# Kernel tuning notes

Hardware: AMD Instinct MI355X
Metric: run time of the kernel (lower is better)

## Reference

```python
import jax, jax.numpy as jnp
import numpy as np
from jax import lax

NPOINT = 1024
RADIUS = 0.4
NSAMPLE = 32
BN_EPS = 1e-5


def _square_distance(src, dst):
    # src [B,S,3], dst [B,N,3] -> [B,S,N]
    d = -2.0 * jnp.einsum('bsc,bnc->bsn', src, dst)
    d = d + jnp.sum(src ** 2, -1)[:, :, None]
    d = d + jnp.sum(dst ** 2, -1)[:, None, :]
    return d


def _farthest_point_sample(xyz, npoint):
    # xyz [B,N,3] -> int32 indices [B,npoint]
    B, N, _ = xyz.shape
    # deterministic start at index 0 (torch uses randint; math is otherwise identical)
    init_far = jnp.zeros((B,), dtype=jnp.int32)
    init_dist = jnp.full((B, N), 1e10, dtype=xyz.dtype)

    def step(carry, _):
        distance, farthest = carry
        centroid = jnp.take_along_axis(xyz, farthest[:, None, None], axis=1)  # [B,1,3]
        dist = jnp.sum((xyz - centroid) ** 2, -1)  # [B,N]
        distance = jnp.minimum(distance, dist)
        new_far = jnp.argmax(distance, axis=-1).astype(jnp.int32)
        return (distance, new_far), farthest

    (_, _), cents = lax.scan(step, (init_dist, init_far), None, length=npoint)
    return cents.T  # [B, npoint]


def _query_ball_point(radius, nsample, xyz, new_xyz):
    # xyz [B,N,3], new_xyz [B,S,3] -> idx [B,S,nsample]
    B, N, _ = xyz.shape
    sqr = _square_distance(new_xyz, xyz)  # [B,S,N]
    ar = jnp.arange(N, dtype=jnp.int32)
    gi = jnp.where(sqr > radius * radius, N, ar[None, None, :])
    gi = jnp.sort(gi, axis=-1)[:, :, :nsample]
    first = gi[:, :, :1]
    return jnp.where(gi == N, first, gi)


def setup_inputs() -> dict:
    key = jax.random.key(0)
    ks = jax.random.split(key, 8)
    B, N = 16, 4096
    inp = {
        'xyz': jax.random.normal(ks[0], (B, 3, N), jnp.float32),
        'points': jax.random.normal(ks[1], (B, 6, N), jnp.float32),
    }
    dims = [(64, 9), (64, 64), (128, 64)]
    for i, (o, c) in enumerate(dims):
        inp[f'w{i}'] = jax.random.normal(ks[2 + i], (o, c), jnp.float32) * 0.05
        inp[f'b{i}'] = jnp.zeros((o,), jnp.float32)
        inp[f'g{i}'] = jnp.ones((o,), jnp.float32)
        inp[f'beta{i}'] = jnp.zeros((o,), jnp.float32)
    return inp


def reference(xyz, points, w0, b0, g0, beta0, w1, b1, g1, beta1, w2, b2, g2, beta2):
    # xyz [B,3,N], points [B,6,N]
    xyz_t = jnp.transpose(xyz, (0, 2, 1))      # [B,N,3]
    pts_t = jnp.transpose(points, (0, 2, 1))   # [B,N,6]
    B, N, _ = xyz_t.shape
    S, ns = NPOINT, NSAMPLE

    fps_idx = _farthest_point_sample(xyz_t, S)                 # [B,S]
    new_xyz = jnp.take_along_axis(xyz_t, fps_idx[:, :, None], axis=1)  # [B,S,3]
    idx = _query_ball_point(RADIUS, ns, xyz_t, new_xyz)        # [B,S,ns]
    flat = idx.reshape(B, S * ns, 1)
    g_xyz = jnp.take_along_axis(xyz_t, flat, axis=1).reshape(B, S, ns, 3)
    g_xyz = g_xyz - new_xyz[:, :, None, :]                     # grouped_xyz_norm
    g_pts = jnp.take_along_axis(pts_t, flat, axis=1).reshape(B, S, ns, -1)
    feat = jnp.concatenate([g_xyz, g_pts], axis=-1)            # [B,S,ns,9]

    # shared MLP: 1x1 conv + BatchNorm (training-mode batch stats) + ReLU
    for w, b, g, be in ((w0, b0, g0, beta0), (w1, b1, g1, beta1), (w2, b2, g2, beta2)):
        h = jnp.einsum('bsnc,oc->bsno', feat, w) + b
        mu = jnp.mean(h, axis=(0, 1, 2))
        var = jnp.var(h, axis=(0, 1, 2))
        feat = jax.nn.relu((h - mu) * lax.rsqrt(var + BN_EPS) * g + be)

    new_points = jnp.max(feat, axis=2)                         # max over nsample -> [B,S,Cout]
    return (jnp.transpose(new_xyz, (0, 2, 1)), jnp.transpose(new_points, (0, 2, 1)))
```

## Files before the change

kernel.cpp:

```cpp
#include <hip/hip_runtime.h>
#include <hip/hip_bf16.h>
#include <stdint.h>

#define NB 16
#define NP 4096
#define NSP 1024
#define KNN 32
#define PTOT (NB*NSP*KNN)
#define NTILES (PTOT/16)

typedef __attribute__((ext_vector_type(8))) short short8;
typedef __attribute__((ext_vector_type(4))) float f32x4;
typedef __attribute__((ext_vector_type(2))) float f32x2;

__device__ __forceinline__ float fadd_(float a,float b){return __fadd_rn(a,b);}
__device__ __forceinline__ float fmul_(float a,float b){return __fmul_rn(a,b);}
__device__ __forceinline__ float fsub_(float a,float b){return __fsub_rn(a,b);}

__device__ __forceinline__ float bf2f(unsigned short u){
    unsigned int x = ((unsigned int)u) << 16; float f; __builtin_memcpy(&f,&x,4); return f;
}
__device__ __forceinline__ unsigned short f2bf(float f){
    unsigned int x; __builtin_memcpy(&x,&f,4);
    x = x + 0x7fffu + ((x>>16)&1u);
    return (unsigned short)(x>>16);
}

template<int CTRL>
__device__ __forceinline__ unsigned long long dpp_max_step(unsigned long long v){
    unsigned int lo = (unsigned int)v, hi = (unsigned int)(v>>32);
    unsigned int lod = (unsigned int)__builtin_amdgcn_update_dpp(0, (int)lo, CTRL, 0xF, 0xF, true);
    unsigned int hid = (unsigned int)__builtin_amdgcn_update_dpp(0, (int)hi, CTRL, 0xF, 0xF, true);
    unsigned long long o = ((unsigned long long)hid<<32) | lod;
    return (o > v) ? o : v;
}

__global__ __launch_bounds__(512,1) void fps_kernel(const float* __restrict__ xyz,
    int* __restrict__ fps_idx)
{
    const int b = blockIdx.x, tid = threadIdx.x;
    const int lane = tid & 63, wv = tid >> 6;
    const float* xb = xyz + (size_t)b*3*NP;
    __shared__ float4 sp[NP];
    __shared__ unsigned long long slots[2][8];
    f32x2 px[4], py[4], pz[4];
    float pd[8];
    const int base = tid*8;
#pragma unroll
    for (int j=0;j<8;j+=4){
        float4 vx = *(const float4*)(xb + base + j);
        float4 vy = *(const float4*)(xb + NP + base + j);
        float4 vz = *(const float4*)(xb + 2*NP + base + j);
        px[j/2]   = (f32x2){vx.x,vx.y}; px[j/2+1] = (f32x2){vx.z,vx.w};
        py[j/2]   = (f32x2){vy.x,vy.y}; py[j/2+1] = (f32x2){vy.z,vy.w};
        pz[j/2]   = (f32x2){vz.x,vz.y}; pz[j/2+1] = (f32x2){vz.z,vz.w};
        sp[base+j+0] = make_float4(vx.x,vy.x,vz.x,0.f);
        sp[base+j+1] = make_float4(vx.y,vy.y,vz.y,0.f);
        sp[base+j+2] = make_float4(vx.z,vy.z,vz.z,0.f);
        sp[base+j+3] = make_float4(vx.w,vy.w,vz.w,0.f);
        pd[j]=1e10f; pd[j+1]=1e10f; pd[j+2]=1e10f; pd[j+3]=1e10f;
    }
    __syncthreads();
    int far = 0;
    float cx, cy, cz;
    { float4 c0 = sp[0]; cx=c0.x; cy=c0.y; cz=c0.z; }
    for (int s=0;s<NSP;s++){
        if (tid==0) fps_idx[b*NSP+s] = far;
        float bd=-1.0f; int bi=0;
        {
#pragma clang fp contract(off)
            const f32x2 cx2 = (f32x2){cx,cx}, cy2 = (f32x2){cy,cy}, cz2 = (f32x2){cz,cz};
#pragma unroll
            for (int k=0;k<4;k++){
                f32x2 dx = px[k]-cx2, dy = py[k]-cy2, dz = pz[k]-cz2;
                f32x2 d  = (dx*dx + dy*dy) + dz*dz;
                float nd0 = fminf(pd[2*k],   d.x);
                float nd1 = fminf(pd[2*k+1], d.y);
                pd[2*k]=nd0; pd[2*k+1]=nd1;
                if (nd0 > bd){ bd=nd0; bi=base+2*k;   }
                if (nd1 > bd){ bd=nd1; bi=base+2*k+1; }
            }
        }
        unsigned int hb; __builtin_memcpy(&hb,&bd,4);
        unsigned long long best = ((unsigned long long)hb<<32) | (unsigned int)(NP-1-bi);
        best = dpp_max_step<0x111>(best);
        best = dpp_max_step<0x112>(best);
        best = dpp_max_step<0x114>(best);
        best = dpp_max_step<0x118>(best);
        best = dpp_max_step<0x142>(best);
        best = dpp_max_step<0x143>(best);
        if (lane==63) slots[s&1][wv] = best;
        __syncthreads();
        {
            const unsigned long long* sl = slots[s&1];
            unsigned long long a0 = sl[0], a1 = sl[1], a2 = sl[2], a3 = sl[3];
            unsigned long long a4 = sl[4], a5 = sl[5], a6 = sl[6], a7 = sl[7];
            unsigned long long m0 = a0>a1?a0:a1, m1 = a2>a3?a2:a3;
            unsigned long long m2 = a4>a5?a4:a5, m3 = a6>a7?a6:a7;
            unsigned long long n0 = m0>m1?m0:m1, n1 = m2>m3?m2:m3;
            unsigned long long m  = n0>n1?n0:n1;
            far = NP-1-(int)(m & 0xFFFFFFFFu);
        }
        float4 c = sp[far]; cx=c.x; cy=c.y; cz=c.z;
    }
}

__global__ void centroid_kernel(const float* __restrict__ xyz, const int* __restrict__ fps_idx,
    float* __restrict__ new_xyz, float* __restrict__ out0)
{
    int t = blockIdx.x*256 + threadIdx.x;
    if (t >= NB*NSP) return;
    int b = t>>10, s = t&1023;
    int id = fps_idx[t];
    const float* xb = xyz + (size_t)b*3*NP;
    float x=xb[id], y=xb[NP+id], z=xb[2*NP+id];
    float* nz = new_xyz + (size_t)t*3;
    nz[0]=x; nz[1]=y; nz[2]=z;
    out0[(size_t)b*3*NSP + s]         = x;
    out0[(size_t)b*3*NSP + NSP + s]   = y;
    out0[(size_t)b*3*NSP + 2*NSP + s] = z;
}

__global__ __launch_bounds__(256,1) void ball_gather_kernel(const float* __restrict__ xyz,
    const float* __restrict__ pts, const float* __restrict__ new_xyz,
    unsigned short* __restrict__ feat)
{
    const int lane = threadIdx.x & 63, wv = threadIdx.x >> 6;
    const int center = blockIdx.x*4 + wv;
    const int b = center >> 10;
    const float* xb = xyz + (size_t)b*3*NP;
    const float* pb = pts + (size_t)b*6*NP;
    const float* nz = new_xyz + (size_t)center*3;
    const float cx=nz[0], cy=nz[1], cz=nz[2];
    const float src2 = fadd_(fadd_(fmul_(cx,cx),fmul_(cy,cy)),fmul_(cz,cz));
    const float R2 = (float)(0.4*0.4);
    __shared__ int slots[4][32];
    int total = 0;
    for (int c0=0;c0<NP;c0+=64){
        const int i = c0 + lane;
        float x=xb[i], y=xb[NP+i], z=xb[2*NP+i];
        float dot  = fadd_(fadd_(fmul_(cx,x),fmul_(cy,y)),fmul_(cz,z));
        float dst2 = fadd_(fadd_(fmul_(x,x),fmul_(y,y)),fmul_(z,z));
        float d = fadd_(fadd_(fmul_(-2.0f,dot), src2), dst2);
        bool pred = !(d > R2);
        unsigned long long m = __ballot(pred);
        int pos = total + (int)__popcll(m & ((1ull<<lane)-1ull));
        if (pred && pos < 32) slots[wv][pos] = i;
        total += (int)__popcll(m);
        if (total >= 32) break;
    }
    const int nvalid = total < 32 ? total : 32;
    const int n = lane & 31;
    const int idx = slots[wv][ (n < nvalid) ? n : 0 ];
    unsigned short* fr = feat + (size_t)center*KNN*32 + (size_t)n*32;
    if (lane < 32){
        float gx = fsub_(xb[idx], cx), gy = fsub_(xb[NP+idx], cy), gz = fsub_(xb[2*NP+idx], cz);
        float p0=pb[idx], p1=pb[NP+idx], p2=pb[2*NP+idx], p3=pb[3*NP+idx], p4=pb[4*NP+idx];
        short8 v;
        v[0]=(short)f2bf(gx); v[1]=(short)f2bf(gy); v[2]=(short)f2bf(gz);
        v[3]=(short)f2bf(p0); v[4]=(short)f2bf(p1); v[5]=(short)f2bf(p2);
        v[6]=(short)f2bf(p3); v[7]=(short)f2bf(p4);
        *(short8*)fr = v;
    } else {
        float p5 = pb[5*NP+idx];
        short8 v = (short8){0,0,0,0,0,0,0,0};
        v[0]=(short)f2bf(p5);
        *(short8*)(fr+8)  = v;
        short8 z8 = (short8){0,0,0,0,0,0,0,0};
        *(short8*)(fr+16) = z8;
        *(short8*)(fr+24) = z8;
    }
}

template<int KT,int OT,bool NORM_IN,bool STORE_H>
__global__ __launch_bounds__(256,1) void conv_kernel(const unsigned short* __restrict__ in,
    const unsigned short* __restrict__ wp, const float* __restrict__ bias,
    const float* __restrict__ nAB, unsigned short* __restrict__ h_out,
    double* __restrict__ stats)
{
    constexpr int K = KT*32, O = OT*16;
    const int lane = threadIdx.x & 63, wv = threadIdx.x >> 6;
    const int col = lane & 15, quad = lane >> 4;
    short8 bf[OT][KT];
#pragma unroll
    for (int t=0;t<OT;t++)
#pragma unroll
        for (int kt=0;kt<KT;kt++)
            bf[t][kt] = *(const short8*)(wp + (size_t)(t*16+col)*K + kt*32 + quad*8);
    float brow[OT];
#pragma unroll
    for (int t=0;t<OT;t++) brow[t] = bias[t*16+col];
    float nA[KT*8], nB[KT*8];
    if constexpr (NORM_IN){
#pragma unroll
        for (int kt=0;kt<KT;kt++)
#pragma unroll
            for (int j=0;j<8;j++){
                int c = kt*32+quad*8+j;
                nA[kt*8+j]=nAB[c]; nB[kt*8+j]=nAB[128+c];
            }
    }
    float ssum[OT], ssq[OT];
#pragma unroll
    for (int t=0;t<OT;t++){ ssum[t]=0.f; ssq[t]=0.f; }
    const int gw = blockIdx.x*4 + wv, nw = gridDim.x*4;
    for (int tile=gw; tile<NTILES; tile+=nw){
        const int row0 = tile*16;
        short8 af[KT];
#pragma unroll
        for (int kt=0;kt<KT;kt++){
            af[kt] = *(const short8*)(in + (size_t)(row0+col)*K + kt*32 + quad*8);
            if constexpr (NORM_IN){
#pragma unroll
                for (int j=0;j<8;j++){
                    float x = bf2f((unsigned short)af[kt][j]);
                    x = fmaxf(x*nA[kt*8+j]+nB[kt*8+j], 0.f);
                    af[kt][j] = (short)f2bf(x);
                }
            }
        }
        f32x4 acc[OT];
#pragma unroll
        for (int t=0;t<OT;t++) acc[t] = (f32x4){0.f,0.f,0.f,0.f};
#pragma unroll
        for (int kt=0;kt<KT;kt++)
#pragma unroll
            for (int t=0;t<OT;t++)
                acc[t] = __builtin_amdgcn_mfma_f32_16x16x32_bf16(af[kt], bf[t][kt], acc[t], 0,0,0);
#pragma unroll
        for (int t=0;t<OT;t++){
#pragma unroll
            for (int r=0;r<4;r++){
                float h = acc[t][r] + brow[t];
                if constexpr (STORE_H)
                    h_out[(size_t)(row0 + quad*4 + r)*O + t*16 + col] = f2bf(h);
                ssum[t] += h; ssq[t] = fmaf(h,h,ssq[t]);
            }
        }
    }
    __shared__ float bsum[128], bssq[128];
    for (int i=threadIdx.x;i<128;i+=256){ bsum[i]=0.f; bssq[i]=0.f; }
    __syncthreads();
#pragma unroll
    for (int t=0;t<OT;t++){
        float v = ssum[t]; v += __shfl_xor(v,16,64); v += __shfl_xor(v,32,64);
        float q = ssq[t];  q += __shfl_xor(q,16,64); q += __shfl_xor(q,32,64);
        if (quad==0){ atomicAdd(&bsum[t*16+col], v); atomicAdd(&bssq[t*16+col], q); }
    }
    __syncthreads();
    if ((int)threadIdx.x < O){
        const int slot = blockIdx.x & 7;
        atomicAdd(&stats[(size_t)(slot*2+0)*128 + threadIdx.x], (double)bsum[threadIdx.x]);
        atomicAdd(&stats[(size_t)(slot*2+1)*128 + threadIdx.x], (double)bssq[threadIdx.x]);
    }
}

__global__ void finalize_kernel(const double* __restrict__ stats, const float* __restrict__ g,
    const float* __restrict__ beta, float* __restrict__ AB, int O)
{
    int o = threadIdx.x;
    if (o >= O) return;
    double s=0.0, q=0.0;
#pragma unroll
    for (int slot=0;slot<8;slot++){
        s += stats[(size_t)(slot*2+0)*128+o];
        q += stats[(size_t)(slot*2+1)*128+o];
    }
    const double cnt = (double)PTOT;
    float mean = (float)(s/cnt);
    float var  = (float)(q/cnt - (s/cnt)*(s/cnt));
    float inv  = rsqrtf(var + 1e-5f);
    float A = g[o]*inv;
    AB[o] = A; AB[128+o] = beta[o] - mean*A;
}

__global__ __launch_bounds__(256,1) void conv_final_kernel(const unsigned short* __restrict__ in,
    const unsigned short* __restrict__ wp, const float* __restrict__ bias,
    const float* __restrict__ nABin, const float* __restrict__ nABout,
    float* __restrict__ out1)
{
    constexpr int KT=2, OT=8, K=64;
    const int lane = threadIdx.x & 63, wv = threadIdx.x >> 6;
    const int col = lane & 15, quad = lane >> 4;
    short8 bf[OT][KT];
#pragma unroll
    for (int t=0;t<OT;t++)
#pragma unroll
        for (int kt=0;kt<KT;kt++)
            bf[t][kt] = *(const short8*)(wp + (size_t)(t*16+col)*K + kt*32 + quad*8);
    float brow[OT], oA[OT], oB[OT];
#pragma unroll
    for (int t=0;t<OT;t++){
        brow[t] = bias[t*16+col];
        oA[t] = nABout[t*16+col];
        oB[t] = nABout[128+t*16+col];
    }
    float nA[16], nB[16];
#pragma unroll
    for (int kt=0;kt<2;kt++)
#pragma unroll
        for (int j=0;j<8;j++){
            int c = kt*32+quad*8+j;
            nA[kt*8+j]=nABin[c]; nB[kt*8+j]=nABin[128+c];
        }
    const int gw = blockIdx.x*4 + wv, nw = gridDim.x*4;
    for (int grp=gw; grp<NB*NSP; grp+=nw){
        float vmax[OT];
#pragma unroll
        for (int t=0;t<OT;t++) vmax[t]=0.f;
#pragma unroll
        for (int mt=0; mt<2; mt++){
            const int row0 = grp*32 + mt*16;
            short8 af[KT];
#pragma unroll
            for (int kt=0;kt<2;kt++){
                af[kt] = *(const short8*)(in + (size_t)(row0+col)*K + kt*32 + quad*8);
#pragma unroll
                for (int j=0;j<8;j++){
                    float x = bf2f((unsigned short)af[kt][j]);
                    x = fmaxf(x*nA[kt*8+j]+nB[kt*8+j], 0.f);
                    af[kt][j] = (short)f2bf(x);
                }
            }
            f32x4 acc[OT];
#pragma unroll
            for (int t=0;t<OT;t++) acc[t] = (f32x4){0.f,0.f,0.f,0.f};
#pragma unroll
            for (int kt=0;kt<2;kt++)
#pragma unroll
                for (int t=0;t<OT;t++)
                    acc[t] = __builtin_amdgcn_mfma_f32_16x16x32_bf16(af[kt], bf[t][kt], acc[t], 0,0,0);
#pragma unroll
            for (int t=0;t<OT;t++){
#pragma unroll
                for (int r=0;r<4;r++){
                    float h = acc[t][r] + brow[t];
                    float x = fmaxf(h*oA[t]+oB[t], 0.f);
                    vmax[t] = fmaxf(vmax[t], x);
                }
            }
        }
#pragma unroll
        for (int t=0;t<OT;t++){
            float v = vmax[t];
            v = fmaxf(v, __shfl_xor(v,16,64));
            v = fmaxf(v, __shfl_xor(v,32,64));
            if (quad==0){
                int o = t*16+col, bb = grp>>10, ss = grp&1023;
                out1[((size_t)bb*128+o)*NSP + ss] = v;
            }
        }
    }
}

__global__ void prep_kernel(const float* __restrict__ w0, const float* __restrict__ w1,
    const float* __restrict__ w2, unsigned short* __restrict__ wp0,
    unsigned short* __restrict__ wp1, unsigned short* __restrict__ wp2)
{
    int t = blockIdx.x*256 + threadIdx.x;
    if (t < 64*32){ int o=t>>5, c=t&31; wp0[t] = (c<9) ? f2bf(w0[o*9+c]) : (unsigned short)0; }
    if (t < 64*64)  wp1[t] = f2bf(w1[t]);
    if (t < 128*64) wp2[t] = f2bf(w2[t]);
}

extern "C" void kernel_launch(void* const* d_in, const int* in_sizes, int n_in,
                              void* d_out, int out_size, void* d_ws, size_t ws_size,
                              hipStream_t stream)
{
    (void)in_sizes; (void)n_in; (void)out_size; (void)ws_size;
    const float* xyz = (const float*)d_in[0];
    const float* pts = (const float*)d_in[1];
    const float* w0  = (const float*)d_in[2];
    const float* b0  = (const float*)d_in[3];
    const float* g0  = (const float*)d_in[4];
    const float* be0 = (const float*)d_in[5];
    const float* w1  = (const float*)d_in[6];
    const float* b1  = (const float*)d_in[7];
    const float* g1  = (const float*)d_in[8];
    const float* be1 = (const float*)d_in[9];
    const float* w2  = (const float*)d_in[10];
    const float* b2  = (const float*)d_in[11];
    const float* g2  = (const float*)d_in[12];
    const float* be2 = (const float*)d_in[13];

    char* ws = (char*)d_ws;
    size_t off = 0;
    auto alloc = [&](size_t sz)->char*{ char* p = ws + off; off = (off + sz + 255) & ~(size_t)255; return p; };
    int*            fps_idx = (int*)           alloc((size_t)NB*NSP*4);
    float*          new_xyz = (float*)         alloc((size_t)NB*NSP*3*4);
    unsigned short* wp0     = (unsigned short*)alloc(64*32*2);
    unsigned short* wp1     = (unsigned short*)alloc(64*64*2);
    unsigned short* wp2     = (unsigned short*)alloc(128*64*2);
    double*         stats   = (double*)        alloc((size_t)3*8*2*128*8);
    float*          AB0     = (float*)         alloc(256*4);
    float*          AB1     = (float*)         alloc(256*4);
    float*          AB2     = (float*)         alloc(256*4);
    unsigned short* feat    = (unsigned short*)alloc((size_t)PTOT*32*2);
    unsigned short* h0      = (unsigned short*)alloc((size_t)PTOT*64*2);
    unsigned short* h1      = (unsigned short*)alloc((size_t)PTOT*64*2);

    float* out0 = (float*)d_out;
    float* out1 = out0 + (size_t)NB*3*NSP;

    hipMemsetAsync(stats, 0, (size_t)3*8*2*128*8, stream);
    prep_kernel<<<32,256,0,stream>>>(w0,w1,w2,wp0,wp1,wp2);
    fps_kernel<<<NB,512,0,stream>>>(xyz, fps_idx);
    centroid_kernel<<<(NB*NSP+255)/256,256,0,stream>>>(xyz, fps_idx, new_xyz, out0);
    ball_gather_kernel<<<NB*NSP/4,256,0,stream>>>(xyz, pts, new_xyz, feat);
    conv_kernel<1,4,false,true><<<1024,256,0,stream>>>(feat, wp0, b0, nullptr, h0, stats);
    finalize_kernel<<<1,128,0,stream>>>(stats, g0, be0, AB0, 64);
    conv_kernel<2,4,true,true><<<1024,256,0,stream>>>(h0, wp1, b1, AB0, h1, stats + 2048);
    finalize_kernel<<<1,128,0,stream>>>(stats + 2048, g1, be1, AB1, 64);
    conv_kernel<2,8,true,false><<<1024,256,0,stream>>>(h1, wp2, b2, AB1, nullptr, stats + 4096);
    finalize_kernel<<<1,128,0,stream>>>(stats + 4096, g2, be2, AB2, 128);
    conv_final_kernel<<<2048,256,0,stream>>>(h1, wp2, b2, AB1, AB2, out1);
}
```

Measured before the change: 889.1 us.

## Restructure FPS argmax as float max-reduce with index recovery, 256 threads

The farthest-point-sampling kernel now uses 256 threads per block, each holding 16 points, instead of 512 threads with 8 points. The per-step argmax no longer carries a 64-bit value/index pair through the DPP reduction. It does a packed-float max reduction, broadcasts the wave max, and recovers the winning index with a compare, ballot and readlane. The intent is to shorten the serial 1024-step loop by cutting reduction work and block sync width, at the cost of more per-thread work and extra index-recovery instructions.

```diff
diff --git a/kernel.cpp b/kernel.cpp
--- a/kernel.cpp
+++ b/kernel.cpp
@@ -27,27 +27,23 @@
 }
 
 template<int CTRL>
-__device__ __forceinline__ unsigned long long dpp_max_step(unsigned long long v){
-    unsigned int lo = (unsigned int)v, hi = (unsigned int)(v>>32);
-    unsigned int lod = (unsigned int)__builtin_amdgcn_update_dpp(0, (int)lo, CTRL, 0xF, 0xF, true);
-    unsigned int hid = (unsigned int)__builtin_amdgcn_update_dpp(0, (int)hi, CTRL, 0xF, 0xF, true);
-    unsigned long long o = ((unsigned long long)hid<<32) | lod;
-    return (o > v) ? o : v;
-}
-
-__global__ __launch_bounds__(512,1) void fps_kernel(const float* __restrict__ xyz,
+__device__ __forceinline__ float dpp_fmax_step(float v){
+    int d = __builtin_amdgcn_update_dpp(0, __float_as_int(v), CTRL, 0xF, 0xF, true);
+    return fmaxf(v, __int_as_float(d));
+}
+
+__global__ __launch_bounds__(256,1) void fps_kernel(const float* __restrict__ xyz,
     int* __restrict__ fps_idx)
 {
     const int b = blockIdx.x, tid = threadIdx.x;
     const int lane = tid & 63, wv = tid >> 6;
     const float* xb = xyz + (size_t)b*3*NP;
     __shared__ float4 sp[NP];
-    __shared__ unsigned long long slots[2][8];
-    f32x2 px[4], py[4], pz[4];
-    float pd[8];
-    const int base = tid*8;
-#pragma unroll
-    for (int j=0;j<8;j+=4){
+    __shared__ unsigned long long slots[2][4];
+    f32x2 px[8], py[8], pz[8], pd2[8];
+    const int base = tid*16;
+#pragma unroll
+    for (int j=0;j<16;j+=4){
         float4 vx = *(const float4*)(xb + base + j);
         float4 vy = *(const float4*)(xb + NP + base + j);
         float4 vz = *(const float4*)(xb + 2*NP + base + j);
@@ -58,7 +54,8 @@
         sp[base+j+1] = make_float4(vx.y,vy.y,vz.y,0.f);
         sp[base+j+2] = make_float4(vx.z,vy.z,vz.z,0.f);
         sp[base+j+3] = make_float4(vx.w,vy.w,vz.w,0.f);
-        pd[j]=1e10f; pd[j+1]=1e10f; pd[j+2]=1e10f; pd[j+3]=1e10f;
+        pd2[j/2]   = (f32x2){1e10f,1e10f};
+        pd2[j/2+1] = (f32x2){1e10f,1e10f};
     }
     __syncthreads();
     int far = 0;
@@ -66,40 +63,46 @@
     { float4 c0 = sp[0]; cx=c0.x; cy=c0.y; cz=c0.z; }
     for (int s=0;s<NSP;s++){
         if (tid==0) fps_idx[b*NSP+s] = far;
-        float bd=-1.0f; int bi=0;
+        f32x2 bm2 = (f32x2){-1.f,-1.f};
         {
 #pragma clang fp contract(off)
             const f32x2 cx2 = (f32x2){cx,cx}, cy2 = (f32x2){cy,cy}, cz2 = (f32x2){cz,cz};
 #pragma unroll
-            for (int k=0;k<4;k++){
+            for (int k=0;k<8;k++){
                 f32x2 dx = px[k]-cx2, dy = py[k]-cy2, dz = pz[k]-cz2;
                 f32x2 d  = (dx*dx + dy*dy) + dz*dz;
-                float nd0 = fminf(pd[2*k],   d.x);
-                float nd1 = fminf(pd[2*k+1], d.y);
-                pd[2*k]=nd0; pd[2*k+1]=nd1;
-                if (nd0 > bd){ bd=nd0; bi=base+2*k;   }
-                if (nd1 > bd){ bd=nd1; bi=base+2*k+1; }
-            }
-        }
-        unsigned int hb; __builtin_memcpy(&hb,&bd,4);
-        unsigned long long best = ((unsigned long long)hb<<32) | (unsigned int)(NP-1-bi);
-        best = dpp_max_step<0x111>(best);
-        best = dpp_max_step<0x112>(best);
-        best = dpp_max_step<0x114>(best);
-        best = dpp_max_step<0x118>(best);
-        best = dpp_max_step<0x142>(best);
-        best = dpp_max_step<0x143>(best);
-        if (lane==63) slots[s&1][wv] = best;
+                pd2[k] = __builtin_elementwise_min(pd2[k], d);
+                bm2    = __builtin_elementwise_max(bm2, pd2[k]);
+            }
+        }
+        float bd = fmaxf(bm2.x, bm2.y);
+        float m = bd;
+        m = dpp_fmax_step<0x111>(m);
+        m = dpp_fmax_step<0x112>(m);
+        m = dpp_fmax_step<0x114>(m);
+        m = dpp_fmax_step<0x118>(m);
+        m = dpp_fmax_step<0x142>(m);
+        m = dpp_fmax_step<0x143>(m);
+        const float wm = __int_as_float(__builtin_amdgcn_readlane(__float_as_int(m), 63));
+        int il = 0;
+#pragma unroll
+        for (int k=7;k>=0;k--){
+            if (pd2[k].y == wm) il = 2*k+1;
+            if (pd2[k].x == wm) il = 2*k;
+        }
+        unsigned long long wmask = __ballot(bd == wm);
+        int L = __ffsll(wmask) - 1;
+        int widx = __builtin_amdgcn_readlane(base + il, L);
+        unsigned long long key = ((unsigned long long)__float_as_uint(wm) << 32)
+                               | (unsigned int)(NP-1-widx);
+        if (lane==0) slots[s&1][wv] = key;
         __syncthreads();
         {
             const unsigned long long* sl = slots[s&1];
             unsigned long long a0 = sl[0], a1 = sl[1], a2 = sl[2], a3 = sl[3];
-            unsigned long long a4 = sl[4], a5 = sl[5], a6 = sl[6], a7 = sl[7];
             unsigned long long m0 = a0>a1?a0:a1, m1 = a2>a3?a2:a3;
-            unsigned long long m2 = a4>a5?a4:a5, m3 = a6>a7?a6:a7;
-            unsigned long long n0 = m0>m1?m0:m1, n1 = m2>m3?m2:m3;
-            unsigned long long m  = n0>n1?n0:n1;
-            far = NP-1-(int)(m & 0xFFFFFFFFu);
+            unsigned long long mm = m0>m1?m0:m1;
+            far = NP-1-(int)(mm & 0xFFFFFFFFu);
         }
         float4 c = sp[far]; cx=c.x; cy=c.y; cz=c.z;
     }
@@ -404,7 +407,7 @@
 
     hipMemsetAsync(stats, 0, (size_t)3*8*2*128*8, stream);
     prep_kernel<<<32,256,0,stream>>>(w0,w1,w2,wp0,wp1,wp2);
-    fps_kernel<<<NB,512,0,stream>>>(xyz, fps_idx);
+    fps_kernel<<<NB,256,0,stream>>>(xyz, fps_idx);
     centroid_kernel<<<(NB*NSP+255)/256,256,0,stream>>>(xyz, fps_idx, new_xyz, out0);
     ball_gather_kernel<<<NB*NSP/4,256,0,stream>>>(xyz, pts, new_xyz, feat);
     conv_kernel<1,4,false,true><<<1024,256,0,stream>>>(feat, wp0, b0, nullptr, h0, stats);
```

After: 882.0 us. Within noise of the previous version (-0.8%).
